# Optimization experiments

Measured on AMD Instinct MI355X. Metric: run time of the kernel, lower is better.

The kernel has to match this reference:

```python
import jax, jax.numpy as jnp
import numpy as np


def _conv(x, w, b, pad):
    # x: (BN, Cin, H, W), w: (Cout, Cin, kh, kw) -> (BN, Cout, H, W)
    y = jax.lax.conv_general_dilated(x, w, window_strides=(1, 1),
                                     padding=[(pad, pad), (pad, pad)],
                                     dimension_numbers=('NCHW', 'OIHW', 'NCHW'))
    return y + b[None, :, None, None]


def setup_inputs() -> dict:
    key = jax.random.key(0)
    ks = jax.random.split(key, 32)
    B, N, H, W = 1, 24, 60, 80
    COR = 4 * (2 * 3 + 1) ** 2 + 1  # 197
    f = jnp.float32

    def p(k, shape, scale=0.02):
        return (jax.random.normal(k, shape, dtype=f) * scale)

    return {
        'net':  jax.random.normal(ks[0], (B, N, 128, H, W), dtype=f),
        'inp':  jax.random.normal(ks[1], (B, N, 128, H, W), dtype=f),
        'corr': jax.random.normal(ks[2], (B, N, COR, H, W), dtype=f),
        'flow': jax.random.normal(ks[3], (B, N, 3, H, W), dtype=f),
        # corr encoder: 1x1 197->128, 3x3 128->128
        'w_ce1': p(ks[4], (128, COR, 1, 1)), 'b_ce1': jnp.zeros((128,), f),
        'w_ce2': p(ks[5], (128, 128, 3, 3)), 'b_ce2': jnp.zeros((128,), f),
        # flow encoder: 7x7 3->128, 3x3 128->64
        'w_fe1': p(ks[6], (128, 3, 7, 7)),   'b_fe1': jnp.zeros((128,), f),
        'w_fe2': p(ks[7], (64, 128, 3, 3)),  'b_fe2': jnp.zeros((64,), f),
        # ConvGRU gates: 3x3 (128 hidden + 320 input = 448) -> 128
        'w_z': p(ks[8], (128, 448, 3, 3)),   'b_z': jnp.zeros((128,), f),
        'w_r': p(ks[9], (128, 448, 3, 3)),   'b_r': jnp.zeros((128,), f),
        'w_q': p(ks[10], (128, 448, 3, 3)),  'b_q': jnp.zeros((128,), f),
        # delta head: 3x3 128->128, 3x3 128->3
        'w_d1': p(ks[11], (128, 128, 3, 3)), 'b_d1': jnp.zeros((128,), f),
        'w_d2': p(ks[12], (3, 128, 3, 3)),   'b_d2': jnp.zeros((3,), f),
        # weight head: 3x3 128->128, 3x3 128->3 (+sigmoid)
        'w_w1': p(ks[13], (128, 128, 3, 3)), 'b_w1': jnp.zeros((128,), f),
        'w_w2': p(ks[14], (3, 128, 3, 3)),   'b_w2': jnp.zeros((3,), f),
    }


def reference(net, inp, corr, flow,
              w_ce1, b_ce1, w_ce2, b_ce2,
              w_fe1, b_fe1, w_fe2, b_fe2,
              w_z, b_z, w_r, b_r, w_q, b_q,
              w_d1, b_d1, w_d2, b_d2,
              w_w1, b_w1, w_w2, b_w2):
    B, N, C, H, W = net.shape
    h = net.reshape(B * N, C, H, W)
    x_inp = inp.reshape(B * N, -1, H, W)
    c = corr.reshape(B * N, -1, H, W)
    fl = flow.reshape(B * N, -1, H, W)

    # correlation encoder
    c = jax.nn.relu(_conv(c, w_ce1, b_ce1, 0))
    c = jax.nn.relu(_conv(c, w_ce2, b_ce2, 1))
    # flow encoder
    fl = jax.nn.relu(_conv(fl, w_fe1, b_fe1, 3))
    fl = jax.nn.relu(_conv(fl, w_fe2, b_fe2, 1))

    # ConvGRU: inputs = cat(inp, corr_feat, flow_feat) -> 320 channels
    x = jnp.concatenate([x_inp, c, fl], axis=1)
    hx = jnp.concatenate([h, x], axis=1)  # 448 ch
    z = jax.nn.sigmoid(_conv(hx, w_z, b_z, 1))
    r = jax.nn.sigmoid(_conv(hx, w_r, b_r, 1))
    q = jnp.tanh(_conv(jnp.concatenate([r * h, x], axis=1), w_q, b_q, 1))
    h = (1.0 - z) * h + z * q

    # heads (GradientClip is identity in forward)
    delta = _conv(jax.nn.relu(_conv(h, w_d1, b_d1, 1)), w_d2, b_d2, 1)
    weight = jax.nn.sigmoid(_conv(jax.nn.relu(_conv(h, w_w1, b_w1, 1)), w_w2, b_w2, 1))

    delta = delta.reshape(B, N, 3, H, W).transpose(0, 1, 3, 4, 2)
    weight = weight.reshape(B, N, 3, H, W).transpose(0, 1, 3, 4, 2)
    net_out = h.reshape(B, N, -1, H, W)
    return (net_out, delta, weight)
```

## Files before the change

kernel.cpp:

```cpp
#include <hip/hip_runtime.h>
#include <stdint.h>
#include <string.h>

#define PXI 4800
#define BNI 24

typedef short bf16x8 __attribute__((ext_vector_type(8)));
typedef float f32x4 __attribute__((ext_vector_type(4)));

__device__ __forceinline__ uint16_t f2b(float f) {
  uint32_t u = __float_as_uint(f);
  u += 0x7fffu + ((u >> 16) & 1u);
  return (uint16_t)(u >> 16);
}
__device__ __forceinline__ float b2f(uint16_t b) {
  return __uint_as_float(((uint32_t)b) << 16);
}
__device__ __forceinline__ float sigm(float x) {
  return 1.0f / (1.0f + __expf(-x));
}

struct SrcDesc {
  const void* p;
  int nstride;
  int coff;
  int pixstride;
  int creal;
  int is_f32;
};

struct ConvParams {
  SrcDesc srcs[14];
  int KS, cog_total, ncb, mode;
  const uint16_t* wpk;
  const float* bias0;
  const float* bias1;
  uint16_t* out0; int ostride0, ochoff0;
  uint16_t* out1; int ostride1, ochoff1;
  const uint16_t* zbuf;
  const uint16_t* hbf;
  const float* netf32;
  float* houtf32;
};

template<int DSPAN, int CW>
__global__ __launch_bounds__(256, 2) void conv_mfma(ConvParams P) {
  constexpr int PAD = (DSPAN - 1) / 2;
  constexpr int NR = 2;
  constexpr int NRS = NR + DSPAN - 1;
  constexpr int UP = 80 + 2 * PAD;
  constexpr int UPITCH = 82 * 64;
  constexpr int NT = DSPAN * DSPAN;
  constexpr int CB = 4 * CW;
  __shared__ __align__(16) uint8_t smem[NRS * UPITCH];
  const int tid = threadIdx.x;
  const int wave = tid >> 6, lane = tid & 63;
  const int bx = blockIdx.x;
  const int total = gridDim.x;
  const int id = (bx & 7) * (total >> 3) + (bx >> 3);
  const int cbk = id % P.ncb;
  const int rg = id / P.ncb;
  const int n = rg / 30, y0 = (rg - n * 30) * NR;
  const int cog0 = cbk * CB + wave * CW;

  f32x4 acc[CW][NR][5];
#pragma unroll
  for (int c = 0; c < CW; ++c)
#pragma unroll
    for (int r = 0; r < NR; ++r)
#pragma unroll
      for (int t = 0; t < 5; ++t)
        acc[c][r][t] = f32x4{0.f, 0.f, 0.f, 0.f};

  const int pxl = lane & 15;
  const int hi16 = (lane >> 4) * 16;
  const int tapstride = P.cog_total * P.KS * 512;
  const uint16_t* wl = P.wpk + lane * 8;

  for (int ks = 0; ks < P.KS; ++ks) {
    __syncthreads();
    const uint16_t* wk0 = wl + ((size_t)cog0 * P.KS + ks) * 512;
    bf16x8 acur[CW];
#pragma unroll
    for (int c = 0; c < CW; ++c)
      acur[c] = *(const bf16x8*)(wk0 + (size_t)c * (P.KS * 512));
    const SrcDesc d = P.srcs[ks];
    if (!d.is_f32) {
      const uint16_t* bp = (const uint16_t*)d.p + (size_t)n * d.nstride + d.coff;
      for (int c = tid; c < NRS * UP * 4; c += 256) {
        int rs = c / (UP * 4);
        int rem = c - rs * (UP * 4);
        int u = rem >> 2, kq = rem & 3;
        int ysrc = y0 + rs - PAD;
        int xs = u - PAD;
        uint4 v; v.x = 0; v.y = 0; v.z = 0; v.w = 0;
        if ((unsigned)ysrc < 60u && (unsigned)xs < 80u)
          v = *(const uint4*)(bp + (size_t)(ysrc * 80 + xs) * d.pixstride + kq * 8);
        *(uint4*)(smem + rs * UPITCH + ((u * 64 + kq * 16) ^ ((u & 7) << 4))) = v;
      }
    } else {
      const int ci = tid >> 3, xg = tid & 7;
      const bool cok = (d.coff + ci) < d.creal;
      const float* fp = (const float*)d.p + (size_t)n * d.nstride +
                        (size_t)(d.coff + ci) * PXI;
#pragma unroll
      for (int rs = 0; rs < NRS; ++rs) {
#pragma unroll
        for (int j = 0; j < 10; ++j) {
          int x = xg + j * 8;
          float v = cok ? fp[(y0 + rs) * 80 + x] : 0.f;
          *(uint16_t*)(smem + rs * UPITCH + ((x * 64 + ci * 2) ^ ((x & 7) << 4))) = f2b(v);
        }
      }
    }
    __syncthreads();
#pragma unroll 1
    for (int tap = 0; tap < NT; ++tap) {
      bf16x8 anx[CW];
      if (tap + 1 < NT) {
        const uint16_t* wn = wk0 + (size_t)(tap + 1) * tapstride;
#pragma unroll
        for (int c = 0; c < CW; ++c)
          anx[c] = *(const bf16x8*)(wn + (size_t)c * (P.KS * 512));
      }
      const int dy = (DSPAN == 3) ? ((tap * 11) >> 5) : 0;
      const int dx = tap - dy * 3;
      const int u0 = pxl + dx;
      const uint8_t* brow = smem + dy * UPITCH + ((u0 * 64 + hi16) ^ ((u0 & 7) << 4));
#pragma unroll
      for (int r = 0; r < NR; ++r) {
#pragma unroll
        for (int t = 0; t < 5; ++t) {
          bf16x8 b = *(const bf16x8*)(brow + r * UPITCH + t * 1024);
#pragma unroll
          for (int c = 0; c < CW; ++c)
            acc[c][r][t] = __builtin_amdgcn_mfma_f32_16x16x32_bf16(acur[c], b, acc[c][r][t], 0, 0, 0);
        }
      }
      if (tap + 1 < NT) {
#pragma unroll
        for (int c = 0; c < CW; ++c)
          acur[c] = anx[c];
      }
    }
  }

  const int rq = lane >> 4;
  for (int c = 0; c < CW; ++c) {
    const int co0 = (cog0 + c) * 16 + rq * 4;
    for (int r = 0; r < NR; ++r) {
      for (int t = 0; t < 5; ++t) {
        const int px = (y0 + r) * 80 + t * 16 + pxl;
        const size_t gpix = (size_t)n * PXI + px;
        float v[4];
#pragma unroll
        for (int rr = 0; rr < 4; ++rr) {
          int co = co0 + rr;
          float bia = (P.bias1 && co >= 128) ? P.bias1[co - 128] : P.bias0[co];
          v[rr] = acc[c][r][t][rr] + bia;
        }
        if (P.mode == 0) {
          uint16_t* op; int cb2;
          if (P.out1 && co0 >= 128) { op = P.out1 + gpix * (size_t)P.ostride1 + P.ochoff1; cb2 = co0 - 128; }
          else                      { op = P.out0 + gpix * (size_t)P.ostride0 + P.ochoff0; cb2 = co0; }
          uint64_t w = 0;
#pragma unroll
          for (int rr = 0; rr < 4; ++rr)
            w |= (uint64_t)f2b(fmaxf(v[rr], 0.f)) << (16 * rr);
          *(uint64_t*)(op + cb2) = w;
        } else if (P.mode == 1) {
          if (co0 < 128) {
            uint64_t w = 0;
#pragma unroll
            for (int rr = 0; rr < 4; ++rr)
              w |= (uint64_t)f2b(sigm(v[rr])) << (16 * rr);
            *(uint64_t*)(P.out0 + gpix * 128 + co0) = w;
          } else {
            uint64_t hw = *(const uint64_t*)(P.hbf + gpix * 448 + (co0 - 128));
            uint64_t w = 0;
#pragma unroll
            for (int rr = 0; rr < 4; ++rr) {
              float rgt = sigm(v[rr]);
              float h = b2f((uint16_t)(hw >> (16 * rr)));
              w |= (uint64_t)f2b(rgt * h) << (16 * rr);
            }
            *(uint64_t*)(P.out1 + gpix * 128 + (co0 - 128)) = w;
          }
        } else {
          uint64_t zw = *(const uint64_t*)(P.zbuf + gpix * 128 + co0);
          uint64_t w = 0;
#pragma unroll
          for (int rr = 0; rr < 4; ++rr) {
            float qv = tanhf(v[rr]);
            float z = b2f((uint16_t)(zw >> (16 * rr)));
            size_t hidx = ((size_t)n * 128 + co0 + rr) * PXI + px;
            float h = P.netf32[hidx];
            float hn = (1.f - z) * h + z * qv;
            P.houtf32[hidx] = hn;
            w |= (uint64_t)f2b(hn) << (16 * rr);
          }
          *(uint64_t*)(P.out0 + gpix * 128 + co0) = w;
        }
      }
    }
  }
}

__global__ __launch_bounds__(256) void nchw2nhwc(const float* src, uint16_t* dst,
                                                 int C, int pixstride, int choff) {
  const int n = blockIdx.y;
  const int px = blockIdx.x * 256 + threadIdx.x;
  if (px >= PXI) return;
  const float* sp = src + (size_t)n * C * PXI + px;
  uint16_t* dp = dst + ((size_t)n * PXI + px) * pixstride + choff;
  for (int c = 0; c < C; c += 8) {
    uint32_t pk[4];
#pragma unroll
    for (int j = 0; j < 4; ++j) {
      uint32_t lo = f2b(sp[(size_t)(c + 2 * j) * PXI]);
      uint32_t hi = f2b(sp[(size_t)(c + 2 * j + 1) * PXI]);
      pk[j] = lo | (hi << 16);
    }
    uint4 v; v.x = pk[0]; v.y = pk[1]; v.z = pk[2]; v.w = pk[3];
    *(uint4*)(dp + c) = v;
  }
}

__global__ __launch_bounds__(256) void im2col_fe1(const float* flow, uint16_t* F2col) {
  __shared__ float tile[3 * 7 * 88];
  __shared__ uint32_t lut[160];
  const int y = blockIdx.x, n = blockIdx.y;
  const int tid = threadIdx.x;
  if (tid < 160) {
    int k = tid;
    if (k < 147) {
      int ci = k / 49, rem = k - ci * 49;
      int ky = rem / 7, kx = rem - ky * 7;
      lut[k] = (uint32_t)ci | ((uint32_t)ky << 8) | ((uint32_t)kx << 16);
    } else lut[k] = 0xFFFFFFFFu;
  }
  for (int c = tid; c < 3 * 7 * 86; c += 256) {
    int ci = c / 602, rem = c - ci * 602;
    int ky = rem / 86, xi = rem - ky * 86;
    int ysrc = y + ky - 3, x = xi - 3;
    float v = 0.f;
    if ((unsigned)ysrc < 60u && (unsigned)x < 80u)
      v = flow[((size_t)(n * 3 + ci) * 60 + ysrc) * 80 + x];
    tile[(ci * 7 + ky) * 88 + xi] = v;
  }
  __syncthreads();
  uint16_t* op = F2col + ((size_t)n * PXI + y * 80) * 160;
  for (int c = tid; c < 80 * 20; c += 256) {
    int px = c / 20, q = c - px * 20;
    int k0 = q * 8;
    uint32_t pk[4];
#pragma unroll
    for (int j = 0; j < 4; ++j) {
      uint16_t w0 = 0, w1 = 0;
      uint32_t l0 = lut[k0 + 2 * j], l1 = lut[k0 + 2 * j + 1];
      if (l0 != 0xFFFFFFFFu)
        w0 = f2b(tile[((l0 & 0xFF) * 7 + ((l0 >> 8) & 0xFF)) * 88 + px + (l0 >> 16)]);
      if (l1 != 0xFFFFFFFFu)
        w1 = f2b(tile[((l1 & 0xFF) * 7 + ((l1 >> 8) & 0xFF)) * 88 + px + (l1 >> 16)]);
      pk[j] = (uint32_t)w0 | ((uint32_t)w1 << 16);
    }
    uint4 v; v.x = pk[0]; v.y = pk[1]; v.z = pk[2]; v.w = pk[3];
    *(uint4*)(op + (size_t)px * 160 + k0) = v;
  }
}

__global__ __launch_bounds__(256) void pack_w(const float* w, uint16_t* wpk,
    int Cout, int Cin, int taps, int CPAD, int cobase, int cogTotal) {
  int idx = blockIdx.x * 256 + threadIdx.x;
  int total = Cout * CPAD * taps;
  if (idx >= total) return;
  int ci = idx % CPAD;
  int rest = idx / CPAD;
  int co = rest % Cout;
  int tap = rest / Cout;
  float v = (ci < Cin) ? w[((size_t)co * Cin + ci) * taps + tap] : 0.f;
  int cog = (cobase + co) >> 4;
  int ks = ci >> 5;
  int lane = ((cobase + co) & 15) | (((ci >> 3) & 3) << 4);
  int KS = CPAD >> 5;
  size_t off = ((size_t)(tap * cogTotal + cog) * KS + ks) * 512 + lane * 8 + (ci & 7);
  wpk[off] = f2b(v);
}

__global__ __launch_bounds__(256) void dw2_kernel(const uint16_t* D1, const uint16_t* W1,
    const float* wd, const float* wwt, const float* bd, const float* bw,
    float* out_delta, float* out_weight) {
  __shared__ float wl[2 * 9 * 3 * 128];
  const int tid = threadIdx.x;
  for (int c = tid; c < 6912; c += 256) {
    int s = c / 3456, rem = c - s * 3456;
    int j = rem / 1152, rem2 = rem - j * 1152;
    int ci = rem2 / 9, tap = rem2 - ci * 9;
    const float* src = s ? wwt : wd;
    wl[((s * 9 + tap) * 3 + j) * 128 + ci] = src[rem];
  }
  __syncthreads();
  int gid = blockIdx.x * 256 + tid;
  if (gid >= BNI * PXI) return;
  int n = gid / PXI, px = gid - n * PXI;
  int y = px / 80, x = px - y * 80;
  float accd[3] = {bd[0], bd[1], bd[2]};
  float accw[3] = {bw[0], bw[1], bw[2]};
  for (int tap = 0; tap < 9; ++tap) {
    int dy = tap / 3, dxm = tap - dy * 3;
    int ys = y + dy - 1, xs = x + dxm - 1;
    if ((unsigned)ys >= 60u || (unsigned)xs >= 80u) continue;
    const uint16_t* dp = D1 + ((size_t)n * PXI + ys * 80 + xs) * 128;
    const uint16_t* wp = W1 + ((size_t)n * PXI + ys * 80 + xs) * 128;
    const float* wtd = &wl[(0 * 9 + tap) * 3 * 128];
    const float* wtw = &wl[(9 + tap) * 3 * 128];
    for (int cq = 0; cq < 16; ++cq) {
      uint4 dv4 = *(const uint4*)(dp + cq * 8);
      uint4 wv4 = *(const uint4*)(wp + cq * 8);
      float dv[8], wv[8];
      const uint32_t* du = (const uint32_t*)&dv4;
      const uint32_t* wu = (const uint32_t*)&wv4;
#pragma unroll
      for (int e = 0; e < 4; ++e) {
        dv[2 * e] = b2f((uint16_t)du[e]); dv[2 * e + 1] = b2f((uint16_t)(du[e] >> 16));
        wv[2 * e] = b2f((uint16_t)wu[e]); wv[2 * e + 1] = b2f((uint16_t)(wu[e] >> 16));
      }
#pragma unroll
      for (int j = 0; j < 3; ++j) {
        f32x4 wa = *(const f32x4*)(wtd + j * 128 + cq * 8);
        f32x4 wb = *(const f32x4*)(wtd + j * 128 + cq * 8 + 4);
        f32x4 va = *(const f32x4*)(wtw + j * 128 + cq * 8);
        f32x4 vb = *(const f32x4*)(wtw + j * 128 + cq * 8 + 4);
#pragma unroll
        for (int e = 0; e < 4; ++e) {
          accd[j] += dv[e] * wa[e] + dv[e + 4] * wb[e];
          accw[j] += wv[e] * va[e] + wv[e + 4] * vb[e];
        }
      }
    }
  }
  size_t ob = ((size_t)n * PXI + px) * 3;
#pragma unroll
  for (int j = 0; j < 3; ++j) {
    out_delta[ob + j] = accd[j];
    out_weight[ob + j] = sigm(accw[j]);
  }
}

extern "C" void kernel_launch(void* const* d_in, const int* in_sizes, int n_in,
                              void* d_out, int out_size, void* d_ws, size_t ws_size,
                              hipStream_t stream) {
  (void)in_sizes; (void)n_in; (void)out_size; (void)ws_size;
  const float* net  = (const float*)d_in[0];
  const float* inp  = (const float*)d_in[1];
  const float* corr = (const float*)d_in[2];
  const float* flow = (const float*)d_in[3];
  const float* w_ce1 = (const float*)d_in[4];   const float* b_ce1 = (const float*)d_in[5];
  const float* w_ce2 = (const float*)d_in[6];   const float* b_ce2 = (const float*)d_in[7];
  const float* w_fe1 = (const float*)d_in[8];   const float* b_fe1 = (const float*)d_in[9];
  const float* w_fe2 = (const float*)d_in[10];  const float* b_fe2 = (const float*)d_in[11];
  const float* w_z  = (const float*)d_in[12];   const float* b_z  = (const float*)d_in[13];
  const float* w_r  = (const float*)d_in[14];   const float* b_r  = (const float*)d_in[15];
  const float* w_q  = (const float*)d_in[16];   const float* b_q  = (const float*)d_in[17];
  const float* w_d1 = (const float*)d_in[18];   const float* b_d1 = (const float*)d_in[19];
  const float* w_d2 = (const float*)d_in[20];   const float* b_d2 = (const float*)d_in[21];
  const float* w_w1 = (const float*)d_in[22];   const float* b_w1 = (const float*)d_in[23];
  const float* w_w2 = (const float*)d_in[24];   const float* b_w2 = (const float*)d_in[25];

  uint8_t* ws = (uint8_t*)d_ws;
  size_t off = 0;
  auto alloc = [&](size_t b) { size_t o = off; off += (b + 255) & ~(size_t)255; return o; };
  uint16_t* wpk_ce1 = (uint16_t*)(ws + alloc(57344));
  uint16_t* wpk_ce2 = (uint16_t*)(ws + alloc(294912));
  uint16_t* wpk_fe1 = (uint16_t*)(ws + alloc(40960));
  uint16_t* wpk_fe2 = (uint16_t*)(ws + alloc(147456));
  uint16_t* wpk_zr  = (uint16_t*)(ws + alloc(2064384));
  uint16_t* wpk_q   = (uint16_t*)(ws + alloc(1032192));
  uint16_t* wpk_dw  = (uint16_t*)(ws + alloc(589824));
  uint16_t* X448 = (uint16_t*)(ws + alloc((size_t)BNI * PXI * 448 * 2));
  uint16_t* C1   = (uint16_t*)(ws + alloc((size_t)BNI * PXI * 128 * 2));
  uint16_t* F1   = (uint16_t*)(ws + alloc((size_t)BNI * PXI * 128 * 2));
  uint16_t* Zb   = (uint16_t*)(ws + alloc((size_t)BNI * PXI * 128 * 2));
  uint16_t* RHb  = (uint16_t*)(ws + alloc((size_t)BNI * PXI * 128 * 2));
  uint16_t* F2col = Zb;

  auto packs = [&](const float* w, uint16_t* dst, int Cout, int Cin, int taps,
                   int CPAD, int cobase, int cogT) {
    int total = Cout * CPAD * taps;
    pack_w<<<(total + 255) / 256, 256, 0, stream>>>(w, dst, Cout, Cin, taps, CPAD, cobase, cogT);
  };
  packs(w_ce1, wpk_ce1, 128, 197, 1, 224, 0, 8);
  packs(w_ce2, wpk_ce2, 128, 128, 9, 128, 0, 8);
  packs(w_fe1, wpk_fe1, 128, 147, 1, 160, 0, 8);
  packs(w_fe2, wpk_fe2, 64, 128, 9, 128, 0, 4);
  packs(w_z,  wpk_zr, 128, 448, 9, 448, 0, 16);
  packs(w_r,  wpk_zr, 128, 448, 9, 448, 128, 16);
  packs(w_q,  wpk_q,  128, 448, 9, 448, 0, 8);
  packs(w_d1, wpk_dw, 128, 128, 9, 128, 0, 16);
  packs(w_w1, wpk_dw, 128, 128, 9, 128, 128, 16);

  nchw2nhwc<<<dim3(19, BNI), 256, 0, stream>>>(net, X448, 128, 448, 0);
  nchw2nhwc<<<dim3(19, BNI), 256, 0, stream>>>(inp, X448, 128, 448, 128);
  im2col_fe1<<<dim3(60, BNI), 256, 0, stream>>>(flow, F2col);

  const int GR = BNI * 30;
  ConvParams p;
  memset(&p, 0, sizeof(p));
  for (int ks = 0; ks < 5; ++ks) p.srcs[ks] = SrcDesc{F2col, PXI * 160, ks * 32, 160, 0, 0};
  p.KS = 5; p.cog_total = 8; p.ncb = 1; p.mode = 0;
  p.wpk = wpk_fe1; p.bias0 = b_fe1;
  p.out0 = F1; p.ostride0 = 128; p.ochoff0 = 0;
  conv_mfma<1, 2><<<GR, 256, 0, stream>>>(p);
  memset(&p, 0, sizeof(p));
  for (int ks = 0; ks < 7; ++ks) p.srcs[ks] = SrcDesc{corr, 197 * PXI, ks * 32, 0, 197, 1};
  p.KS = 7; p.cog_total = 8; p.ncb = 1; p.mode = 0;
  p.wpk = wpk_ce1; p.bias0 = b_ce1;
  p.out0 = C1; p.ostride0 = 128; p.ochoff0 = 0;
  conv_mfma<1, 2><<<GR, 256, 0, stream>>>(p);
  memset(&p, 0, sizeof(p));
  for (int ks = 0; ks < 4; ++ks) p.srcs[ks] = SrcDesc{C1, PXI * 128, ks * 32, 128, 0, 0};
  p.KS = 4; p.cog_total = 8; p.ncb = 1; p.mode = 0;
  p.wpk = wpk_ce2; p.bias0 = b_ce2;
  p.out0 = X448; p.ostride0 = 448; p.ochoff0 = 256;
  conv_mfma<3, 2><<<GR, 256, 0, stream>>>(p);
  memset(&p, 0, sizeof(p));
  for (int ks = 0; ks < 4; ++ks) p.srcs[ks] = SrcDesc{F1, PXI * 128, ks * 32, 128, 0, 0};
  p.KS = 4; p.cog_total = 4; p.ncb = 1; p.mode = 0;
  p.wpk = wpk_fe2; p.bias0 = b_fe2;
  p.out0 = X448; p.ostride0 = 448; p.ochoff0 = 384;
  conv_mfma<3, 1><<<GR, 256, 0, stream>>>(p);
  memset(&p, 0, sizeof(p));
  for (int ks = 0; ks < 14; ++ks) p.srcs[ks] = SrcDesc{X448, PXI * 448, ks * 32, 448, 0, 0};
  p.KS = 14; p.cog_total = 16; p.ncb = 2; p.mode = 1;
  p.wpk = wpk_zr; p.bias0 = b_z; p.bias1 = b_r;
  p.out0 = Zb; p.out1 = RHb; p.hbf = X448;
  conv_mfma<3, 2><<<GR * 2, 256, 0, stream>>>(p);
  memset(&p, 0, sizeof(p));
  for (int ks = 0; ks < 4; ++ks)  p.srcs[ks] = SrcDesc{RHb, PXI * 128, ks * 32, 128, 0, 0};
  for (int ks = 4; ks < 14; ++ks) p.srcs[ks] = SrcDesc{X448, PXI * 448, 128 + (ks - 4) * 32, 448, 0, 0};
  p.KS = 14; p.cog_total = 8; p.ncb = 1; p.mode = 2;
  p.wpk = wpk_q; p.bias0 = b_q;
  p.out0 = C1; p.zbuf = Zb; p.netf32 = net; p.houtf32 = (float*)d_out;
  conv_mfma<3, 2><<<GR, 256, 0, stream>>>(p);
  memset(&p, 0, sizeof(p));
  for (int ks = 0; ks < 4; ++ks) p.srcs[ks] = SrcDesc{C1, PXI * 128, ks * 32, 128, 0, 0};
  p.KS = 4; p.cog_total = 16; p.ncb = 2; p.mode = 0;
  p.wpk = wpk_dw; p.bias0 = b_d1; p.bias1 = b_w1;
  p.out0 = Zb; p.ostride0 = 128; p.ochoff0 = 0;
  p.out1 = RHb; p.ostride1 = 128; p.ochoff1 = 0;
  conv_mfma<3, 2><<<GR * 2, 256, 0, stream>>>(p);
  float* dout = (float*)d_out;
  dw2_kernel<<<450, 256, 0, stream>>>(Zb, RHb, w_d2, w_w2, b_d2, b_w2,
                                      dout + 14745600, dout + 15091200);
}
```

Measured before the change: 928.2 us.

## Double-buffer LDS input tiles and prefetch next K-slice into registers

The conv kernel now keeps two shared-memory buffers. It issues the global loads for the next input-channel slice into registers before running the MFMA tap loop on the current buffer, then writes them to the other buffer afterward. One barrier per slice replaces two, and global load latency is meant to overlap with matrix compute. In exchange it doubles LDS use, which with launch_bounds(256,2) could lower occupancy, and it holds many extra VGPRs for the staged values, which risks spills. The f32 source path still stages synchronously into the other buffer.

```diff
diff --git a/kernel.cpp b/kernel.cpp
--- a/kernel.cpp
+++ b/kernel.cpp
@@ -52,7 +52,9 @@
   constexpr int UPITCH = 82 * 64;
   constexpr int NT = DSPAN * DSPAN;
   constexpr int CB = 4 * CW;
-  __shared__ __align__(16) uint8_t smem[NRS * UPITCH];
+  constexpr int TOT = NRS * UP * 4;
+  constexpr int NLD = (TOT + 255) / 256;
+  __shared__ __align__(16) uint8_t smem[2][NRS * UPITCH];
   const int tid = threadIdx.x;
   const int wave = tid >> 6, lane = tid & 63;
   const int bx = blockIdx.x;
@@ -77,17 +79,12 @@
   const int tapstride = P.cog_total * P.KS * 512;
   const uint16_t* wl = P.wpk + lane * 8;
 
-  for (int ks = 0; ks < P.KS; ++ks) {
-    __syncthreads();
-    const uint16_t* wk0 = wl + ((size_t)cog0 * P.KS + ks) * 512;
-    bf16x8 acur[CW];
-#pragma unroll
-    for (int c = 0; c < CW; ++c)
-      acur[c] = *(const bf16x8*)(wk0 + (size_t)c * (P.KS * 512));
-    const SrcDesc d = P.srcs[ks];
+  auto stage_inline = [&](int ksi, int buf) {
+    const SrcDesc d = P.srcs[ksi];
+    uint8_t* sb = smem[buf];
     if (!d.is_f32) {
       const uint16_t* bp = (const uint16_t*)d.p + (size_t)n * d.nstride + d.coff;
-      for (int c = tid; c < NRS * UP * 4; c += 256) {
+      for (int c = tid; c < TOT; c += 256) {
         int rs = c / (UP * 4);
         int rem = c - rs * (UP * 4);
         int u = rem >> 2, kq = rem & 3;
@@ -96,7 +93,7 @@
         uint4 v; v.x = 0; v.y = 0; v.z = 0; v.w = 0;
         if ((unsigned)ysrc < 60u && (unsigned)xs < 80u)
           v = *(const uint4*)(bp + (size_t)(ysrc * 80 + xs) * d.pixstride + kq * 8);
-        *(uint4*)(smem + rs * UPITCH + ((u * 64 + kq * 16) ^ ((u & 7) << 4))) = v;
+        *(uint4*)(sb + rs * UPITCH + ((u * 64 + kq * 16) ^ ((u & 7) << 4))) = v;
       }
     } else {
       const int ci = tid >> 3, xg = tid & 7;
@@ -109,11 +106,52 @@
         for (int j = 0; j < 10; ++j) {
           int x = xg + j * 8;
           float v = cok ? fp[(y0 + rs) * 80 + x] : 0.f;
-          *(uint16_t*)(smem + rs * UPITCH + ((x * 64 + ci * 2) ^ ((x & 7) << 4))) = f2b(v);
+          *(uint16_t*)(sb + rs * UPITCH + ((x * 64 + ci * 2) ^ ((x & 7) << 4))) = f2b(v);
         }
       }
     }
-    __syncthreads();
+  };
+
+  stage_inline(0, 0);
+  __syncthreads();
+
+  for (int ks = 0; ks < P.KS; ++ks) {
+    const int cur = ks & 1, nxt = cur ^ 1;
+    const uint16_t* wk0 = wl + ((size_t)cog0 * P.KS + ks) * 512;
+    bf16x8 acur[CW];
+#pragma unroll
+    for (int c = 0; c < CW; ++c)
+      acur[c] = *(const bf16x8*)(wk0 + (size_t)c * (P.KS * 512));
+
+    uint4 sv[NLD];
+    int ldsoff[NLD];
+    bool regged = false;
+    if (ks + 1 < P.KS) {
+      const SrcDesc d = P.srcs[ks + 1];
+      if (!d.is_f32) {
+        const uint16_t* bp = (const uint16_t*)d.p + (size_t)n * d.nstride + d.coff;
+#pragma unroll
+        for (int i = 0; i < NLD; ++i) {
+          int c = tid + i * 256;
+          sv[i].x = 0; sv[i].y = 0; sv[i].z = 0; sv[i].w = 0;
+          ldsoff[i] = 0;
+          if (c < TOT) {
+            int rs = c / (UP * 4);
+            int rem = c - rs * (UP * 4);
+            int u = rem >> 2, kq = rem & 3;
+            int ysrc = y0 + rs - PAD;
+            int xs = u - PAD;
+            ldsoff[i] = rs * UPITCH + ((u * 64 + kq * 16) ^ ((u & 7) << 4));
+            if ((unsigned)ysrc < 60u && (unsigned)xs < 80u)
+              sv[i] = *(const uint4*)(bp + (size_t)(ysrc * 80 + xs) * d.pixstride + kq * 8);
+          }
+        }
+        regged = true;
+      } else {
+        stage_inline(ks + 1, nxt);
+      }
+    }
+
 #pragma unroll 1
     for (int tap = 0; tap < NT; ++tap) {
       bf16x8 anx[CW];
@@ -126,7 +164,7 @@
       const int dy = (DSPAN == 3) ? ((tap * 11) >> 5) : 0;
       const int dx = tap - dy * 3;
       const int u0 = pxl + dx;
-      const uint8_t* brow = smem + dy * UPITCH + ((u0 * 64 + hi16) ^ ((u0 & 7) << 4));
+      const uint8_t* brow = smem[cur] + dy * UPITCH + ((u0 * 64 + hi16) ^ ((u0 & 7) << 4));
 #pragma unroll
       for (int r = 0; r < NR; ++r) {
 #pragma unroll
@@ -143,6 +181,16 @@
           acur[c] = anx[c];
       }
     }
+
+    if (regged) {
+      uint8_t* sb = smem[nxt];
+#pragma unroll
+      for (int i = 0; i < NLD; ++i) {
+        int c = tid + i * 256;
+        if (c < TOT) *(uint4*)(sb + ldsoff[i]) = sv[i];
+      }
+    }
+    __syncthreads();
   }
 
   const int rq = lane >> 4;
```

Measured after the change: 1.033 ms. 1.11x slower.

## Store intermediate activations in zero-bordered padded layout to drop halo bounds checks

Applied to the files above, without the earlier changes.

Intermediate NHWC bf16 buffers (X448, C1, F1, RHb) now use a 62x82 padded spatial layout with zeroed borders. The 3x3 conv staging loads then read halos without per-element bounds checks or zero fills. Producers write into the padded interior, and small kernels zero the borders. This adds extra launches and a slightly larger memory footprint, and it reuses X448 as the w1 output buffer, so correctness depends on the ordering of buffer reuse.

```diff
diff --git a/kernel.cpp b/kernel.cpp
--- a/kernel.cpp
+++ b/kernel.cpp
@@ -3,6 +3,7 @@
 #include <string.h>
 
 #define PXI 4800
+#define NPAD 5084
 #define BNI 24
 
 typedef short bf16x8 __attribute__((ext_vector_type(8)));
@@ -27,11 +28,13 @@
   int pixstride;
   int creal;
   int is_f32;
+  int padded;
 };
 
 struct ConvParams {
   SrcDesc srcs[14];
   int KS, cog_total, ncb, mode;
+  int opad0, opad1;
   const uint16_t* wpk;
   const float* bias0;
   const float* bias1;
@@ -85,7 +88,16 @@
     for (int c = 0; c < CW; ++c)
       acur[c] = *(const bf16x8*)(wk0 + (size_t)c * (P.KS * 512));
     const SrcDesc d = P.srcs[ks];
-    if (!d.is_f32) {
+    if (d.padded) {
+      const uint16_t* bp = (const uint16_t*)d.p + (size_t)n * d.nstride + d.coff;
+      for (int c = tid; c < NRS * UP * 4; c += 256) {
+        int rs = c / (UP * 4);
+        int rem = c - rs * (UP * 4);
+        int u = rem >> 2, kq = rem & 3;
+        uint4 v = *(const uint4*)(bp + (size_t)((y0 + rs) * 82 + u) * d.pixstride + kq * 8);
+        *(uint4*)(smem + rs * UPITCH + ((u * 64 + kq * 16) ^ ((u & 7) << 4))) = v;
+      }
+    } else if (!d.is_f32) {
       const uint16_t* bp = (const uint16_t*)d.p + (size_t)n * d.nstride + d.coff;
       for (int c = tid; c < NRS * UP * 4; c += 256) {
         int rs = c / (UP * 4);
@@ -150,8 +162,10 @@
     const int co0 = (cog0 + c) * 16 + rq * 4;
     for (int r = 0; r < NR; ++r) {
       for (int t = 0; t < 5; ++t) {
-        const int px = (y0 + r) * 80 + t * 16 + pxl;
-        const size_t gpix = (size_t)n * PXI + px;
+        const int Y = y0 + r, X = t * 16 + pxl;
+        const int px = Y * 80 + X;
+        const size_t gpu = (size_t)n * PXI + px;
+        const size_t gpp = (size_t)n * NPAD + (Y + 1) * 82 + (X + 1);
         float v[4];
 #pragma unroll
         for (int rr = 0; rr < 4; ++rr) {
@@ -161,8 +175,13 @@
         }
         if (P.mode == 0) {
           uint16_t* op; int cb2;
-          if (P.out1 && co0 >= 128) { op = P.out1 + gpix * (size_t)P.ostride1 + P.ochoff1; cb2 = co0 - 128; }
-          else                      { op = P.out0 + gpix * (size_t)P.ostride0 + P.ochoff0; cb2 = co0; }
+          if (P.out1 && co0 >= 128) {
+            op = P.out1 + (P.opad1 ? gpp : gpu) * (size_t)P.ostride1 + P.ochoff1;
+            cb2 = co0 - 128;
+          } else {
+            op = P.out0 + (P.opad0 ? gpp : gpu) * (size_t)P.ostride0 + P.ochoff0;
+            cb2 = co0;
+          }
           uint64_t w = 0;
 #pragma unroll
           for (int rr = 0; rr < 4; ++rr)
@@ -174,9 +193,9 @@
 #pragma unroll
             for (int rr = 0; rr < 4; ++rr)
               w |= (uint64_t)f2b(sigm(v[rr])) << (16 * rr);
-            *(uint64_t*)(P.out0 + gpix * 128 + co0) = w;
+            *(uint64_t*)(P.out0 + gpu * 128 + co0) = w;
           } else {
-            uint64_t hw = *(const uint64_t*)(P.hbf + gpix * 448 + (co0 - 128));
+            uint64_t hw = *(const uint64_t*)(P.hbf + gpp * 448 + (co0 - 128));
             uint64_t w = 0;
 #pragma unroll
             for (int rr = 0; rr < 4; ++rr) {
@@ -184,10 +203,10 @@
               float h = b2f((uint16_t)(hw >> (16 * rr)));
               w |= (uint64_t)f2b(rgt * h) << (16 * rr);
             }
-            *(uint64_t*)(P.out1 + gpix * 128 + (co0 - 128)) = w;
+            *(uint64_t*)(P.out1 + gpp * 128 + (co0 - 128)) = w;
           }
         } else {
-          uint64_t zw = *(const uint64_t*)(P.zbuf + gpix * 128 + co0);
+          uint64_t zw = *(const uint64_t*)(P.zbuf + gpu * 128 + co0);
           uint64_t w = 0;
 #pragma unroll
           for (int rr = 0; rr < 4; ++rr) {
@@ -199,11 +218,25 @@
             P.houtf32[hidx] = hn;
             w |= (uint64_t)f2b(hn) << (16 * rr);
           }
-          *(uint64_t*)(P.out0 + gpix * 128 + co0) = w;
+          *(uint64_t*)(P.out0 + (P.opad0 ? gpp : gpu) * 128 + co0) = w;
         }
       }
     }
   }
+}
+
+__global__ __launch_bounds__(256) void zero_borders(uint16_t* buf, int CS) {
+  int vecs = CS >> 3;
+  int idx = blockIdx.x * 256 + threadIdx.x;
+  int tot = BNI * 284 * vecs;
+  if (idx >= tot) return;
+  int v = idx % vecs; int rest = idx / vecs;
+  int b = rest % 284; int n = rest / 284;
+  int r, c;
+  if (b < 164) { r = (b < 82) ? 0 : 61; c = (b < 82) ? b : b - 82; }
+  else { int b2 = b - 164; r = 1 + (b2 % 60); c = (b2 < 60) ? 0 : 81; }
+  uint4 z; z.x = 0; z.y = 0; z.z = 0; z.w = 0;
+  *(uint4*)(buf + ((size_t)n * NPAD + r * 82 + c) * CS + v * 8) = z;
 }
 
 __global__ __launch_bounds__(256) void nchw2nhwc(const float* src, uint16_t* dst,
@@ -212,7 +245,7 @@
   const int px = blockIdx.x * 256 + threadIdx.x;
   if (px >= PXI) return;
   const float* sp = src + (size_t)n * C * PXI + px;
-  uint16_t* dp = dst + ((size_t)n * PXI + px) * pixstride + choff;
+  uint16_t* dp = dst + ((size_t)n * NPAD + (px / 80 + 1) * 82 + (px % 80 + 1)) * pixstride + choff;
   for (int c = 0; c < C; c += 8) {
     uint32_t pk[4];
 #pragma unroll
@@ -377,12 +410,13 @@
   uint16_t* wpk_zr  = (uint16_t*)(ws + alloc(2064384));
   uint16_t* wpk_q   = (uint16_t*)(ws + alloc(1032192));
   uint16_t* wpk_dw  = (uint16_t*)(ws + alloc(589824));
-  uint16_t* X448 = (uint16_t*)(ws + alloc((size_t)BNI * PXI * 448 * 2));
-  uint16_t* C1   = (uint16_t*)(ws + alloc((size_t)BNI * PXI * 128 * 2));
-  uint16_t* F1   = (uint16_t*)(ws + alloc((size_t)BNI * PXI * 128 * 2));
+  uint16_t* X448 = (uint16_t*)(ws + alloc((size_t)BNI * NPAD * 448 * 2));
+  uint16_t* C1   = (uint16_t*)(ws + alloc((size_t)BNI * NPAD * 128 * 2));
+  uint16_t* F1   = (uint16_t*)(ws + alloc((size_t)BNI * NPAD * 128 * 2));
   uint16_t* Zb   = (uint16_t*)(ws + alloc((size_t)BNI * PXI * 128 * 2));
-  uint16_t* RHb  = (uint16_t*)(ws + alloc((size_t)BNI * PXI * 128 * 2));
+  uint16_t* RHb  = (uint16_t*)(ws + alloc((size_t)BNI * NPAD * 128 * 2));
   uint16_t* F2col = Zb;
+  uint16_t* W1buf = X448;
 
   auto packs = [&](const float* w, uint16_t* dst, int Cout, int Cin, int taps,
                    int CPAD, int cobase, int cogT) {
@@ -399,6 +433,10 @@
   packs(w_d1, wpk_dw, 128, 128, 9, 128, 0, 16);
   packs(w_w1, wpk_dw, 128, 128, 9, 128, 128, 16);
 
+  zero_borders<<<(BNI * 284 * 56 + 255) / 256, 256, 0, stream>>>(X448, 448);
+  zero_borders<<<(BNI * 284 * 16 + 255) / 256, 256, 0, stream>>>(C1, 128);
+  zero_borders<<<(BNI * 284 * 16 + 255) / 256, 256, 0, stream>>>(F1, 128);
+
   nchw2nhwc<<<dim3(19, BNI), 256, 0, stream>>>(net, X448, 128, 448, 0);
   nchw2nhwc<<<dim3(19, BNI), 256, 0, stream>>>(inp, X448, 128, 448, 128);
   im2col_fe1<<<dim3(60, BNI), 256, 0, stream>>>(flow, F2col);
@@ -406,50 +444,51 @@
   const int GR = BNI * 30;
   ConvParams p;
   memset(&p, 0, sizeof(p));
-  for (int ks = 0; ks < 5; ++ks) p.srcs[ks] = SrcDesc{F2col, PXI * 160, ks * 32, 160, 0, 0};
-  p.KS = 5; p.cog_total = 8; p.ncb = 1; p.mode = 0;
+  for (int ks = 0; ks < 5; ++ks) p.srcs[ks] = SrcDesc{F2col, PXI * 160, ks * 32, 160, 0, 0, 0};
+  p.KS = 5; p.cog_total = 8; p.ncb = 1; p.mode = 0; p.opad0 = 1;
   p.wpk = wpk_fe1; p.bias0 = b_fe1;
   p.out0 = F1; p.ostride0 = 128; p.ochoff0 = 0;
   conv_mfma<1, 2><<<GR, 256, 0, stream>>>(p);
-  memset(&p, 0, sizeof(p));
-  for (int ks = 0; ks < 7; ++ks) p.srcs[ks] = SrcDesc{corr, 197 * PXI, ks * 32, 0, 197, 1};
-  p.KS = 7; p.cog_total = 8; p.ncb = 1; p.mode = 0;
+  zero_borders<<<(BNI * 284 * 16 + 255) / 256, 256, 0, stream>>>(RHb, 128);
+  memset(&p, 0, sizeof(p));
+  for (int ks = 0; ks < 7; ++ks) p.srcs[ks] = SrcDesc{corr, 197 * PXI, ks * 32, 0, 197, 1, 0};
+  p.KS = 7; p.cog_total = 8; p.ncb = 1; p.mode = 0; p.opad0 = 1;
   p.wpk = wpk_ce1; p.bias0 = b_ce1;
   p.out0 = C1; p.ostride0 = 128; p.ochoff0 = 0;
   conv_mfma<1, 2><<<GR, 256, 0, stream>>>(p);
   memset(&p, 0, sizeof(p));
-  for (int ks = 0; ks < 4; ++ks) p.srcs[ks] = SrcDesc{C1, PXI * 128, ks * 32, 128, 0, 0};
-  p.KS = 4; p.cog_total = 8; p.ncb = 1; p.mode = 0;
+  for (int ks = 0; ks < 4; ++ks) p.srcs[ks] = SrcDesc{C1, NPAD * 128, ks * 32, 128, 0, 0, 1};
+  p.KS = 4; p.cog_total = 8; p.ncb = 1; p.mode = 0; p.opad0 = 1;
   p.wpk = wpk_ce2; p.bias0 = b_ce2;
   p.out0 = X448; p.ostride0 = 448; p.ochoff0 = 256;
   conv_mfma<3, 2><<<GR, 256, 0, stream>>>(p);
   memset(&p, 0, sizeof(p));
-  for (int ks = 0; ks < 4; ++ks) p.srcs[ks] = SrcDesc{F1, PXI * 128, ks * 32, 128, 0, 0};
-  p.KS = 4; p.cog_total = 4; p.ncb = 1; p.mode = 0;
+  for (int ks = 0; ks < 4; ++ks) p.srcs[ks] = SrcDesc{F1, NPAD * 128, ks * 32, 128, 0, 0, 1};
+  p.KS = 4; p.cog_total = 4; p.ncb = 1; p.mode = 0; p.opad0 = 1;
   p.wpk = wpk_fe2; p.bias0 = b_fe2;
   p.out0 = X448; p.ostride0 = 448; p.ochoff0 = 384;
   conv_mfma<3, 1><<<GR, 256, 0, stream>>>(p);
   memset(&p, 0, sizeof(p));
-  for (int ks = 0; ks < 14; ++ks) p.srcs[ks] = SrcDesc{X448, PXI * 448, ks * 32, 448, 0, 0};
-  p.KS = 14; p.cog_total = 16; p.ncb = 2; p.mode = 1;
+  for (int ks = 0; ks < 14; ++ks) p.srcs[ks] = SrcDesc{X448, NPAD * 448, ks * 32, 448, 0, 0, 1};
+  p.KS = 14; p.cog_total = 16; p.ncb = 2; p.mode = 1; p.opad1 = 1;
   p.wpk = wpk_zr; p.bias0 = b_z; p.bias1 = b_r;
   p.out0 = Zb; p.out1 = RHb; p.hbf = X448;
   conv_mfma<3, 2><<<GR * 2, 256, 0, stream>>>(p);
   memset(&p, 0, sizeof(p));
-  for (int ks = 0; ks < 4; ++ks)  p.srcs[ks] = SrcDesc{RHb, PXI * 128, ks * 32, 128, 0, 0};
-  for (int ks = 4; ks < 14; ++ks) p.srcs[ks] = SrcDesc{X448, PXI * 448, 128 + (ks - 4) * 32, 448, 0, 0};
-  p.KS = 14; p.cog_total = 8; p.ncb = 1; p.mode = 2;
+  for (int ks = 0; ks < 4; ++ks)  p.srcs[ks] = SrcDesc{RHb, NPAD * 128, ks * 32, 128, 0, 0, 1};
+  for (int ks = 4; ks < 14; ++ks) p.srcs[ks] = SrcDesc{X448, NPAD * 448, 128 + (ks - 4) * 32, 448, 0, 0, 1};
+  p.KS = 14; p.cog_total = 8; p.ncb = 1; p.mode = 2; p.opad0 = 1;
   p.wpk = wpk_q; p.bias0 = b_q;
   p.out0 = C1; p.zbuf = Zb; p.netf32 = net; p.houtf32 = (float*)d_out;
   conv_mfma<3, 2><<<GR, 256, 0, stream>>>(p);
   memset(&p, 0, sizeof(p));
-  for (int ks = 0; ks < 4; ++ks) p.srcs[ks] = SrcDesc{C1, PXI * 128, ks * 32, 128, 0, 0};
+  for (int ks = 0; ks < 4; ++ks) p.srcs[ks] = SrcDesc{C1, NPAD * 128, ks * 32, 128, 0, 0, 1};
   p.KS = 4; p.cog_total = 16; p.ncb = 2; p.mode = 0;
   p.wpk = wpk_dw; p.bias0 = b_d1; p.bias1 = b_w1;
   p.out0 = Zb; p.ostride0 = 128; p.ochoff0 = 0;
-  p.out1 = RHb; p.ostride1 = 128; p.ochoff1 = 0;
+  p.out1 = W1buf; p.ostride1 = 128; p.ochoff1 = 0;
   conv_mfma<3, 2><<<GR * 2, 256, 0, stream>>>(p);
   float* dout = (float*)d_out;
-  dw2_kernel<<<450, 256, 0, stream>>>(Zb, RHb, w_d2, w_w2, b_d2, b_w2,
+  dw2_kernel<<<450, 256, 0, stream>>>(Zb, W1buf, w_d2, w_w2, b_d2, b_w2,
                                       dout + 14745600, dout + 15091200);
 }
```

New measurement: 1.152 ms. 1.24x slower.
